# Kernel optimization log

Measured on AMD Instinct MI355X. Metric: run time of the kernel, lower is better.

The kernel has to match this reference:

```python
import jax, jax.numpy as jnp
import numpy as np

N = 100000      # nodes
E = 3200000     # edges (avg degree 32)
DIN, DH, DOUT = 128, 32, 2


def setup_inputs() -> dict:
    key = jax.random.key(0)
    k1, k2, k3, k4 = jax.random.split(key, 4)
    x = jax.random.normal(k1, (N, DIN), dtype=jnp.float32)
    edge_index = jax.random.randint(k2, (2, E), 0, N, dtype=jnp.int64)
    # Glorot-ish scaled weights
    W1 = jax.random.normal(k3, (DIN, DH), dtype=jnp.float32) / np.sqrt(DIN)
    b1 = jnp.zeros((DH,), dtype=jnp.float32)
    W2 = jax.random.normal(k4, (DH, DOUT), dtype=jnp.float32) / np.sqrt(DH)
    b2 = jnp.zeros((DOUT,), dtype=jnp.float32)
    return {"x": x, "edge_index": edge_index, "W1": W1, "b1": b1, "W2": W2, "b2": b2}


def reference(x, edge_index, W1, b1, W2, b2):
    n = x.shape[0]
    # GCNConv default: add self-loops, symmetric deg^{-1/2} A deg^{-1/2} normalization
    loops = jnp.arange(n, dtype=edge_index.dtype)
    src = jnp.concatenate([edge_index[0], loops])  # [E+N]
    dst = jnp.concatenate([edge_index[1], loops])  # [E+N]
    deg = jax.ops.segment_sum(jnp.ones_like(dst, dtype=x.dtype), dst, num_segments=n)
    dinv = jnp.where(deg > 0, jax.lax.rsqrt(deg), 0.0)
    norm = dinv[src] * dinv[dst]  # [E+N]

    def gcn_layer(h, W, b):
        m = h @ W                                   # [n, dout] transform first (PyG order)
        msgs = m[src] * norm[:, None]               # gather + scale  [E+N, dout]
        agg = jax.ops.segment_sum(msgs, dst, num_segments=n)  # scatter-add
        return agg + b

    h = jax.nn.relu(gcn_layer(x, W1, b1))
    return gcn_layer(h, W2, b2)
```

## Files before the change

### kernel.cpp

```cpp
#include <hip/hip_runtime.h>
#include <hip/hip_bf16.h>

#define DIN 128
#define DH 32
#define DOUT 2
#define NPB 128
#define NPB_SHIFT 7
#define NBUK_MAX 1024
#define FILL_EDGES 8192
#define ECHUNK 2048
#define CAP 5632

#define FXS1 2048.0f
#define FXI1 (1.0f / 2048.0f)
#define FXS2 131072.0f
#define FXI2 (1.0f / 131072.0f)


__device__ inline int sxlo(unsigned int w) { return (int)(short)(w & 0xFFFFu); }
__device__ inline int sxhi(unsigned int w) { return ((int)w) >> 16; }

__global__ void zero_kernel(int* __restrict__ gcur, int nbuk,
                            unsigned int* __restrict__ mqrow) {
    int i = blockIdx.x * blockDim.x + threadIdx.x;
    if (i < nbuk) gcur[i] = 0;
    if (blockIdx.x == 0 && threadIdx.x < 16) mqrow[threadIdx.x] = 0u;
}

__global__ void binfill_kernel(const int* __restrict__ src, const int* __restrict__ dst,
                               int* __restrict__ gcur, unsigned int* __restrict__ binned,
                               int e, int nbuk) {
    __shared__ int cnt[NBUK_MAX];
    __shared__ int pos[NBUK_MAX];
    __shared__ int gb[NBUK_MAX];
    __shared__ unsigned int sorted[FILL_EDGES];
    __shared__ unsigned short aux[FILL_EDGES];
    __shared__ int stmp[256];

    int t = threadIdx.x;
    int e0 = blockIdx.x * FILL_EDGES;
    int m = min(FILL_EDGES, e - e0);

    for (int i = t; i < nbuk; i += 256) cnt[i] = 0;
    __syncthreads();
    for (int i = t; i < m; i += 256) atomicAdd(&cnt[dst[e0 + i] >> NPB_SHIFT], 1);
    __syncthreads();

    int v[4], s = 0;
#pragma unroll
    for (int k = 0; k < 4; ++k) {
        int i = 4 * t + k;
        v[k] = (i < nbuk) ? cnt[i] : 0;
        s += v[k];
    }
    stmp[t] = s;
    __syncthreads();
    for (int off = 1; off < 256; off <<= 1) {
        int x = (t >= off) ? stmp[t - off] : 0;
        __syncthreads();
        stmp[t] += x;
        __syncthreads();
    }
    int run = stmp[t] - s;
#pragma unroll
    for (int k = 0; k < 4; ++k) {
        int i = 4 * t + k;
        if (i < nbuk) pos[i] = run;
        run += v[k];
    }
    __syncthreads();

    for (int i = t; i < m; i += 256) {
        int d = dst[e0 + i];
        int sv = src[e0 + i];
        int b = d >> NPB_SHIFT;
        int r = atomicAdd(&pos[b], 1);
        sorted[r] = ((unsigned int)(d & (NPB - 1)) << 17) | (unsigned int)sv;
        aux[r] = (unsigned short)b;
    }
    __syncthreads();

    for (int b = t; b < nbuk; b += 256) {
        int c = cnt[b];
        gb[b] = c ? atomicAdd(&gcur[b], c) : 0;
    }
    __syncthreads();

    for (int i = t; i < m; i += 256) {
        int b = aux[i];
        int start = pos[b] - cnt[b];
        unsigned int off = (unsigned int)(gb[b] + (i - start));
        if (off < (unsigned int)CAP)
            binned[(size_t)b * CAP + off] = sorted[i];
    }
}

__global__ void bdinv_kernel(const int* __restrict__ gcur,
                             const unsigned int* __restrict__ binned,
                             float* __restrict__ dinv, int n) {
    __shared__ int cnt[NPB];
    int t = threadIdx.x;
    int b = blockIdx.x;
    if (t < NPB) cnt[t] = 0;
    __syncthreads();
    const unsigned int* bp = binned + (size_t)b * CAP;
    const int cntb = min(gcur[b], CAP);
    for (int i = t; i < cntb; i += 256) atomicAdd(&cnt[bp[i] >> 17], 1);
    __syncthreads();
    if (t < NPB) {
        int r = (b << NPB_SHIFT) + t;
        if (r < n) dinv[r] = rsqrtf((float)(cnt[t] + 1));
    }
}

#define XTS 68
__global__ void __launch_bounds__(128, 4)
gemm1_kernel(const float* __restrict__ x, const float* __restrict__ W1,
             const float* __restrict__ dinv,
             short* __restrict__ mqc, int n) {
    __shared__ float  XT[DIN * XTS];
    __shared__ float4 Wl4[DIN * 8];

    int t = threadIdx.x;
    for (int i = t; i < DIN * 8; i += 128) Wl4[i] = ((const float4*)W1)[i];

    int rb = blockIdx.x * 64;
    for (int i = t; i < 64 * 32; i += 128) {
        int r = i & 63, kq = i >> 6;
        int gr = rb + r;
        float4 v = make_float4(0.f, 0.f, 0.f, 0.f);
        if (gr < n) v = ((const float4*)x)[(size_t)gr * 32 + kq];
        XT[(4 * kq + 0) * XTS + r] = v.x;
        XT[(4 * kq + 1) * XTS + r] = v.y;
        XT[(4 * kq + 2) * XTS + r] = v.z;
        XT[(4 * kq + 3) * XTS + r] = v.w;
    }
    __syncthreads();

    const int cq = t & 7;
    const int rq = t >> 3;
    float4 a0 = make_float4(0.f, 0.f, 0.f, 0.f);
    float4 a1 = a0, a2 = a0, a3 = a0;
#pragma unroll 8
    for (int k = 0; k < DIN; ++k) {
        float4 xv = *(const float4*)&XT[k * XTS + 4 * rq];
        float4 w  = Wl4[k * 8 + cq];
        a0.x += xv.x * w.x; a0.y += xv.x * w.y; a0.z += xv.x * w.z; a0.w += xv.x * w.w;
        a1.x += xv.y * w.x; a1.y += xv.y * w.y; a1.z += xv.y * w.z; a1.w += xv.y * w.w;
        a2.x += xv.z * w.x; a2.y += xv.z * w.y; a2.z += xv.z * w.z; a2.w += xv.z * w.w;
        a3.x += xv.w * w.x; a3.y += xv.w * w.y; a3.z += xv.w * w.z; a3.w += xv.w * w.w;
    }
#pragma unroll
    for (int m = 0; m < 4; ++m) {
        int r = rb + 4 * rq + m;
        if (r < n) {
            float di = dinv[r] * FXS1;
            float4 av = (m == 0) ? a0 : (m == 1) ? a1 : (m == 2) ? a2 : a3;
            short4 sv;
            sv.x = (short)__float2int_rn(av.x * di);
            sv.y = (short)__float2int_rn(av.y * di);
            sv.z = (short)__float2int_rn(av.z * di);
            sv.w = (short)__float2int_rn(av.w * di);
            *(short4*)&mqc[(size_t)r * DH + 4 * cq] = sv;
        }
    }
}

__global__ void __launch_bounds__(512, 8)
agg1_kernel(const int* __restrict__ gcur,
            const unsigned int* __restrict__ binned,
            const short* __restrict__ mqc,
            const float* __restrict__ dinv,
            const float* __restrict__ b1, const float* __restrict__ W2,
            float2* __restrict__ m2q, int n) {
    __shared__ int acc[NPB * 33];
    __shared__ unsigned int ebuf[2][ECHUNK];

    const int t = threadIdx.x;
    const int b = blockIdx.x;
    const int cntb = min(gcur[b], CAP);
    const int r0 = b << NPB_SHIFT;

    for (int i = t; i < NPB * 33; i += 512) acc[i] = 0;

    const unsigned int* __restrict__ bp = binned + (size_t)b * CAP;
    const unsigned int* __restrict__ mq32 = (const unsigned int*)mqc;
    const unsigned int sent = (unsigned int)n;
    const int nchunks = (cntb + ECHUNK - 1) / ECHUNK;

    unsigned int st[4];
    if (nchunks > 0) {
#pragma unroll
        for (int k = 0; k < 4; ++k) {
            int idx = t + k * 512;
            st[k] = (idx < cntb) ? __builtin_nontemporal_load(&bp[idx]) : sent;
        }
#pragma unroll
        for (int k = 0; k < 4; ++k) ebuf[0][t + k * 512] = st[k];
    }
    __syncthreads();

    const int g = t >> 4, l = t & 15;

    for (int c = 0; c < nchunks; ++c) {
        if (c + 1 < nchunks) {
            const int base = (c + 1) * ECHUNK;
#pragma unroll
            for (int k = 0; k < 4; ++k) {
                int idx = base + t + k * 512;
                st[k] = (idx < cntb) ? __builtin_nontemporal_load(&bp[idx]) : sent;
            }
        }
        const unsigned int* eb = ebuf[c & 1];
        for (int j = 0; j < 64; j += 8) {
            const unsigned int* ej = &eb[g + 32 * j];
            unsigned int e0 = ej[0],   e1 = ej[32],  e2 = ej[64],  e3 = ej[96];
            unsigned int e4 = ej[128], e5 = ej[160], e6 = ej[192], e7 = ej[224];
            unsigned int w0 = mq32[(e0 & 0x1FFFFu) * 16u + l];
            unsigned int w1 = mq32[(e1 & 0x1FFFFu) * 16u + l];
            unsigned int w2 = mq32[(e2 & 0x1FFFFu) * 16u + l];
            unsigned int w3 = mq32[(e3 & 0x1FFFFu) * 16u + l];
            unsigned int w4 = mq32[(e4 & 0x1FFFFu) * 16u + l];
            unsigned int w5 = mq32[(e5 & 0x1FFFFu) * 16u + l];
            unsigned int w6 = mq32[(e6 & 0x1FFFFu) * 16u + l];
            unsigned int w7 = mq32[(e7 & 0x1FFFFu) * 16u + l];
            int d0 = (int)(e0 >> 17) * 33 + 2 * l;
            int d1 = (int)(e1 >> 17) * 33 + 2 * l;
            int d2 = (int)(e2 >> 17) * 33 + 2 * l;
            int d3 = (int)(e3 >> 17) * 33 + 2 * l;
            int d4 = (int)(e4 >> 17) * 33 + 2 * l;
            int d5 = (int)(e5 >> 17) * 33 + 2 * l;
            int d6 = (int)(e6 >> 17) * 33 + 2 * l;
            int d7 = (int)(e7 >> 17) * 33 + 2 * l;
            atomicAdd(&acc[d0], sxlo(w0)); atomicAdd(&acc[d0 + 1], sxhi(w0));
            atomicAdd(&acc[d1], sxlo(w1)); atomicAdd(&acc[d1 + 1], sxhi(w1));
            atomicAdd(&acc[d2], sxlo(w2)); atomicAdd(&acc[d2 + 1], sxhi(w2));
            atomicAdd(&acc[d3], sxlo(w3)); atomicAdd(&acc[d3 + 1], sxhi(w3));
            atomicAdd(&acc[d4], sxlo(w4)); atomicAdd(&acc[d4 + 1], sxhi(w4));
            atomicAdd(&acc[d5], sxlo(w5)); atomicAdd(&acc[d5 + 1], sxhi(w5));
            atomicAdd(&acc[d6], sxlo(w6)); atomicAdd(&acc[d6 + 1], sxhi(w6));
            atomicAdd(&acc[d7], sxlo(w7)); atomicAdd(&acc[d7 + 1], sxhi(w7));
        }
        __syncthreads();
        if (c + 1 < nchunks) {
#pragma unroll
            for (int k = 0; k < 4; ++k) ebuf[(c + 1) & 1][t + k * 512] = st[k];
        }
        __syncthreads();
    }

    const int j = t >> 2, q = t & 3;
    const int r = r0 + j;
    if (r < n) {
        const float di = dinv[r];
        const unsigned int* srow = (const unsigned int*)mqc + (size_t)r * 16 + q * 4;
        const int* ar = &acc[j * 33 + q * 8];
        float p0 = 0.f, p1 = 0.f;
#pragma unroll
        for (int k = 0; k < 4; ++k) {
            unsigned int sw = srow[k];
            int c = q * 8 + 2 * k;
            float h0 = fmaxf(di * (float)(ar[2 * k]     + sxlo(sw)) * FXI1 + b1[c],     0.0f);
            float h1 = fmaxf(di * (float)(ar[2 * k + 1] + sxhi(sw)) * FXI1 + b1[c + 1], 0.0f);
            p0 += h0 * W2[2 * c]     + h1 * W2[2 * c + 2];
            p1 += h0 * W2[2 * c + 1] + h1 * W2[2 * c + 3];
        }
        p0 += __shfl_down(p0, 2, 4); p0 += __shfl_down(p0, 1, 4);
        p1 += __shfl_down(p1, 2, 4); p1 += __shfl_down(p1, 1, 4);
        if (q == 0) m2q[r] = make_float2(di * p0, di * p1);
    }
}

__global__ void __launch_bounds__(256, 4)
agg2_kernel(const int* __restrict__ gcur,
            const unsigned int* __restrict__ binned,
            const float2* __restrict__ m2q,
            const float* __restrict__ dinv, const float* __restrict__ b2,
            float* __restrict__ out, int n) {
    __shared__ int a0s[NPB], a1s[NPB];
    const int t = threadIdx.x;
    const int b = blockIdx.x;
    const int cntb = min(gcur[b], CAP);
    const int r0 = b << NPB_SHIFT;

    if (t < NPB) { a0s[t] = 0; a1s[t] = 0; }
    __syncthreads();

    const unsigned int* __restrict__ bp = binned + (size_t)b * CAP;
    int i = t;
    for (; i + 768 < cntb; i += 1024) {
        unsigned int e0 = __builtin_nontemporal_load(&bp[i]);
        unsigned int e1 = __builtin_nontemporal_load(&bp[i + 256]);
        unsigned int e2 = __builtin_nontemporal_load(&bp[i + 512]);
        unsigned int e3 = __builtin_nontemporal_load(&bp[i + 768]);
        float2 v0 = m2q[e0 & 0x1FFFFu];
        float2 v1 = m2q[e1 & 0x1FFFFu];
        float2 v2 = m2q[e2 & 0x1FFFFu];
        float2 v3 = m2q[e3 & 0x1FFFFu];
        atomicAdd(&a0s[e0 >> 17], __float2int_rn(v0.x * FXS2));
        atomicAdd(&a1s[e0 >> 17], __float2int_rn(v0.y * FXS2));
        atomicAdd(&a0s[e1 >> 17], __float2int_rn(v1.x * FXS2));
        atomicAdd(&a1s[e1 >> 17], __float2int_rn(v1.y * FXS2));
        atomicAdd(&a0s[e2 >> 17], __float2int_rn(v2.x * FXS2));
        atomicAdd(&a1s[e2 >> 17], __float2int_rn(v2.y * FXS2));
        atomicAdd(&a0s[e3 >> 17], __float2int_rn(v3.x * FXS2));
        atomicAdd(&a1s[e3 >> 17], __float2int_rn(v3.y * FXS2));
    }
    for (; i < cntb; i += 256) {
        unsigned int e0 = __builtin_nontemporal_load(&bp[i]);
        float2 v0 = m2q[e0 & 0x1FFFFu];
        atomicAdd(&a0s[e0 >> 17], __float2int_rn(v0.x * FXS2));
        atomicAdd(&a1s[e0 >> 17], __float2int_rn(v0.y * FXS2));
    }
    __syncthreads();

    if (t < NPB) {
        int r = r0 + t;
        if (r < n) {
            float di = dinv[r];
            float2 self = m2q[r];
            out[(size_t)r * DOUT + 0] = di * ((float)a0s[t] * FXI2 + self.x) + b2[0];
            out[(size_t)r * DOUT + 1] = di * ((float)a1s[t] * FXI2 + self.y) + b2[1];
        }
    }
}

extern "C" void kernel_launch(void* const* d_in, const int* in_sizes, int n_in,
                              void* d_out, int out_size, void* d_ws, size_t ws_size,
                              hipStream_t stream) {
    const float* x  = (const float*)d_in[0];
    const int*   ei = (const int*)d_in[1];
    const float* W1 = (const float*)d_in[2];
    const float* b1 = (const float*)d_in[3];
    const float* W2 = (const float*)d_in[4];
    const float* b2 = (const float*)d_in[5];
    float* out = (float*)d_out;

    const int n = in_sizes[0] / DIN;
    const int e = in_sizes[1] / 2;
    const int* src = ei;
    const int* dst = ei + e;
    const int nbuk = (n + NPB - 1) >> NPB_SHIFT;

    char* ws = (char*)d_ws;
    float* dinv   = (float*)ws;          ws += (size_t)n * 4;
    int* gcur     = (int*)ws;            ws += NBUK_MAX * 4;
    unsigned int* binned = (unsigned int*)ws;   ws += (size_t)nbuk * CAP * 4;
    short* mqc    = (short*)ws;          ws += ((size_t)n + 1) * DH * 2;
    float2* m2q   = (float2*)ws;

    const int B = 256;
    const int fill_blocks = (e + FILL_EDGES - 1) / FILL_EDGES;

    zero_kernel<<<(nbuk + B - 1) / B, B, 0, stream>>>(
        gcur, nbuk, (unsigned int*)(mqc + (size_t)n * DH));
    binfill_kernel<<<fill_blocks, B, 0, stream>>>(src, dst, gcur, binned, e, nbuk);
    bdinv_kernel<<<nbuk, B, 0, stream>>>(gcur, binned, dinv, n);
    gemm1_kernel<<<(n + 63) / 64, 128, 0, stream>>>(x, W1, dinv, mqc, n);
    agg1_kernel<<<nbuk, 512, 0, stream>>>(gcur, binned, mqc, dinv, b1, W2, m2q, n);
    agg2_kernel<<<nbuk, B, 0, stream>>>(gcur, binned, m2q, dinv, b2, out, n);
}
```

Before: 236.4 us.

## Simplify bin fill: drop LDS sort and scan, write directly with atomic offsets

The bin-fill kernel no longer stages edges in a shared-memory sorted buffer with a prefix scan. Each block counts edges per bucket, reserves global offsets right away, and then writes each edge straight to global memory at a shared-atomic offset. Blocks grow to 1024 threads, one per bucket, and shared memory use drops, so more blocks can be resident. The trade-off is that global writes are no longer grouped into contiguous runs per bucket, so store coalescing may get worse. Order within each bucket also becomes nondeterministic.

```diff
diff --git a/kernel.cpp b/kernel.cpp
--- a/kernel.cpp
+++ b/kernel.cpp
@@ -27,71 +27,37 @@
     if (blockIdx.x == 0 && threadIdx.x < 16) mqrow[threadIdx.x] = 0u;
 }
 
-__global__ void binfill_kernel(const int* __restrict__ src, const int* __restrict__ dst,
-                               int* __restrict__ gcur, unsigned int* __restrict__ binned,
-                               int e, int nbuk) {
-    __shared__ int cnt[NBUK_MAX];
+__global__ void __launch_bounds__(1024, 2)
+binfill_kernel(const int* __restrict__ src, const int* __restrict__ dst,
+               int* __restrict__ gcur, unsigned int* __restrict__ binned,
+               int e, int nbuk) {
+    __shared__ int lcnt[NBUK_MAX];
     __shared__ int pos[NBUK_MAX];
     __shared__ int gb[NBUK_MAX];
-    __shared__ unsigned int sorted[FILL_EDGES];
-    __shared__ unsigned short aux[FILL_EDGES];
-    __shared__ int stmp[256];
 
     int t = threadIdx.x;
     int e0 = blockIdx.x * FILL_EDGES;
     int m = min(FILL_EDGES, e - e0);
 
-    for (int i = t; i < nbuk; i += 256) cnt[i] = 0;
-    __syncthreads();
-    for (int i = t; i < m; i += 256) atomicAdd(&cnt[dst[e0 + i] >> NPB_SHIFT], 1);
-    __syncthreads();
-
-    int v[4], s = 0;
-#pragma unroll
-    for (int k = 0; k < 4; ++k) {
-        int i = 4 * t + k;
-        v[k] = (i < nbuk) ? cnt[i] : 0;
-        s += v[k];
-    }
-    stmp[t] = s;
-    __syncthreads();
-    for (int off = 1; off < 256; off <<= 1) {
-        int x = (t >= off) ? stmp[t - off] : 0;
-        __syncthreads();
-        stmp[t] += x;
-        __syncthreads();
-    }
-    int run = stmp[t] - s;
-#pragma unroll
-    for (int k = 0; k < 4; ++k) {
-        int i = 4 * t + k;
-        if (i < nbuk) pos[i] = run;
-        run += v[k];
-    }
-    __syncthreads();
-
-    for (int i = t; i < m; i += 256) {
+    if (t < nbuk) lcnt[t] = 0;
+    __syncthreads();
+    for (int i = t; i < m; i += 1024) atomicAdd(&lcnt[dst[e0 + i] >> NPB_SHIFT], 1);
+    __syncthreads();
+    if (t < nbuk) {
+        int c = lcnt[t];
+        int g = c ? atomicAdd(&gcur[t], c) : 0;
+        gb[t] = g;
+        pos[t] = g;
+    }
+    __syncthreads();
+    for (int i = t; i < m; i += 1024) {
         int d = dst[e0 + i];
         int sv = src[e0 + i];
         int b = d >> NPB_SHIFT;
-        int r = atomicAdd(&pos[b], 1);
-        sorted[r] = ((unsigned int)(d & (NPB - 1)) << 17) | (unsigned int)sv;
-        aux[r] = (unsigned short)b;
-    }
-    __syncthreads();
-
-    for (int b = t; b < nbuk; b += 256) {
-        int c = cnt[b];
-        gb[b] = c ? atomicAdd(&gcur[b], c) : 0;
-    }
-    __syncthreads();
-
-    for (int i = t; i < m; i += 256) {
-        int b = aux[i];
-        int start = pos[b] - cnt[b];
-        unsigned int off = (unsigned int)(gb[b] + (i - start));
+        unsigned int off = (unsigned int)atomicAdd(&pos[b], 1);
         if (off < (unsigned int)CAP)
-            binned[(size_t)b * CAP + off] = sorted[i];
+            binned[(size_t)b * CAP + off] =
+                ((unsigned int)(d & (NPB - 1)) << 17) | (unsigned int)sv;
     }
 }
 
@@ -354,7 +320,7 @@
 
     zero_kernel<<<(nbuk + B - 1) / B, B, 0, stream>>>(
         gcur, nbuk, (unsigned int*)(mqc + (size_t)n * DH));
-    binfill_kernel<<<fill_blocks, B, 0, stream>>>(src, dst, gcur, binned, e, nbuk);
+    binfill_kernel<<<fill_blocks, 1024, 0, stream>>>(src, dst, gcur, binned, e, nbuk);
     bdinv_kernel<<<nbuk, B, 0, stream>>>(gcur, binned, dinv, n);
     gemm1_kernel<<<(n + 63) / 64, 128, 0, stream>>>(x, W1, dinv, mqc, n);
     agg1_kernel<<<nbuk, 512, 0, stream>>>(gcur, binned, mqc, dinv, b1, W2, m2q, n);
```

After: 239.2 us. No clear change (+1.2%).
